# Performance work log

Hardware: AMD Instinct MI355X
Metric: run time of the kernel (lower is better)

The kernel has to match this reference:

```python
import jax, jax.numpy as jnp
import numpy as np

RADIUS = 0.08       # float radius -> patches_radius float branch
K = 32              # patch_size_source; spacing = 0 so topk k == K


def setup_inputs() -> dict:
    key = jax.random.key(0)
    k1, k2, k3, k4 = jax.random.split(key, 4)
    B, Ns, Nt = 2, 2048, 32768  # Nt = 32**3 (perfect cube for H_t reshape)
    return {
        "source": jax.random.normal(k1, (B, Ns, 3), dtype=jnp.float32),
        "target": jax.random.normal(k2, (B, Nt, 3), dtype=jnp.float32),
        "source_density": jax.random.uniform(k3, (B, Ns, 1), dtype=jnp.float32),
        "target_density": jax.random.uniform(k4, (B, Nt, 1), dtype=jnp.float32),
    }


def reference(source, target, source_density, target_density):
    B, Ns, _ = source.shape
    Nt = target.shape[1]

    # pairwise squared distances: (B, Nt, Ns)
    r0 = jnp.sum(target * target, axis=2, keepdims=True)            # B,Nt,1
    r1 = jnp.sum(source * source, axis=2, keepdims=True)            # B,Ns,1
    sq_dist = r0 - 2.0 * jnp.einsum('btc,bsc->bts', target, source) + jnp.swapaxes(r1, 1, 2)

    # computed in the original forward but never used downstream (dead value)
    _sq_dist_sel = sq_dist / (jnp.einsum('bti,bsi->bts', target_density, source_density) + 1e-8)

    # top-k nearest neighbors (spacing == 0)
    neg_vals, idx = jax.lax.top_k(-sq_dist, K)                      # B,Nt,K
    sq_pd = -neg_vals

    rad = RADIUS * jnp.ones((B, 1, 1), dtype=sq_dist.dtype)
    valid = (rad ** 2) >= sq_pd                                     # B,Nt,K (rad broadcast)
    idx = jnp.where(valid, idx, -1)

    b_idx = jnp.arange(B)[:, None, None]                            # B,1,1
    src_s = source / (rad + 1e-6)
    tgt_s = target / (rad + 1e-6)

    safe = jnp.maximum(idx, 0)
    patches = jnp.where(valid[..., None], src_s[b_idx, safe], 0.0)  # B,Nt,K,3
    patches = patches - tgt_s[:, :, None, :]
    density = jnp.where(valid[..., None], source_density[b_idx, safe], 0.0)  # B,Nt,K,1

    # gather of an all-ones (B,Ns) mask == validity indicator
    patch_valid = valid.astype(patches.dtype)
    patches_size = jnp.sum(patch_valid, axis=-1)                    # B,Nt

    patches_dist = jnp.sqrt(jnp.maximum(sq_pd, 1e-9)) / (rad + 1e-6)  # B,Nt,K

    mask_cnt = jnp.sum((idx < 0).astype(jnp.int32), axis=-1, keepdims=True)  # B,Nt,1
    weight_density = jnp.sum(density, axis=-2) / mask_cnt            # B,Nt,1

    H = int(round(Nt ** (1.0 / 3.0)))
    patches_idx = jnp.stack([jnp.broadcast_to(b_idx, (B, Nt, K)), idx], axis=-1)

    return (
        patches.reshape(B, H, H, H, K, 3),        # patches source
        patches_idx.reshape(B, H, H, H, K, 2),    # patches idx source
        patches_size,                              # patches size source
        rad,                                       # patches radius source
        patches_dist.reshape(B, H, H, H, K),       # patches dist source
        weight_density,                            # weighted density
    )
```

## Files before the change

kernel.cpp:

```cpp
#include <hip/hip_runtime.h>
#include <math.h>

constexpr int B_  = 2;
constexpr int NS_ = 2048;
constexpr int NT_ = 32768;
constexpr int K_  = 32;
#define RADIUS_F 0.08f

constexpr int TPB = 512;
constexpr int TGT_PER_WAVE = 8;
constexpr int TGT_PER_BLOCK = 8 * TGT_PER_WAVE;
constexpr int BLOCKS_PER_BATCH = NT_ / TGT_PER_BLOCK;
constexpr int NCHUNK = NS_ / 64;

constexpr int SZ_PATCH = B_ * NT_ * K_ * 3;
constexpr int SZ_IDX   = B_ * NT_ * K_ * 2;
constexpr int SZ_SIZE  = B_ * NT_;
constexpr int SZ_RAD   = B_;
constexpr int SZ_DIST  = B_ * NT_ * K_;
constexpr int O_PATCH = 0;
constexpr int O_IDX   = O_PATCH + SZ_PATCH;
constexpr int O_SIZE  = O_IDX + SZ_IDX;
constexpr int O_RAD   = O_SIZE + SZ_SIZE;
constexpr int O_DIST  = O_RAD + SZ_RAD;
constexpr int O_WD    = O_DIST + SZ_DIST;

constexpr unsigned long long tm_mask(int k, int j) {
    unsigned long long m = 0;
    for (int l = 0; l < 64; ++l)
        if (((l & k) == 0) == ((l & j) == 0)) m |= 1ull << l;
    return m;
}

__device__ __forceinline__ float readlane_f(float v, int l) {
    return __int_as_float(__builtin_amdgcn_readlane(__float_as_int(v), l));
}
__device__ __forceinline__ float bperm_f(int addr, float v) {
    return __int_as_float(__builtin_amdgcn_ds_bpermute(addr, __float_as_int(v)));
}
__device__ __forceinline__ float shr1_f(float v) {
    return __int_as_float(__builtin_amdgcn_update_dpp(0, __float_as_int(v),
                                                      0x138, 0xF, 0xF, true));
}
__device__ __forceinline__ float med3_vsv(float pv, int vbits, float lv) {
    float r;
    asm("v_med3_f32 %0, %1, %2, %3" : "=v"(r) : "v"(pv), "s"(vbits), "v"(lv));
    return r;
}
__device__ __forceinline__ float maxs_f(float p, int wbits) {
    float r;
    asm("v_max_f32 %0, %1, %2" : "=v"(r) : "s"(wbits), "v"(p));
    return r;
}
__device__ __forceinline__ float min3_f(float a, float b, float c) {
    float r;
    asm("v_min3_f32 %0, %1, %2, %3" : "=v"(r) : "v"(a), "v"(b), "v"(c));
    return r;
}
__device__ __forceinline__ void cnds(float& lv, float pv, unsigned long long keep) {
    float r;
    asm("v_cndmask_b32 %0, %2, %1, %3" : "=v"(r) : "v"(lv), "v"(pv), "s"(keep));
    lv = r;
}
__device__ __forceinline__ float dist_f(float tx, float ty, float tz, float r0, float4 sp) {
    float dot2 = __fadd_rn(__fadd_rn(__fmul_rn(tx, sp.x), __fmul_rn(ty, sp.y)), __fmul_rn(tz, sp.z));
    return __fadd_rn(__fadd_rn(r0, dot2), sp.w);
}

#define BSTG(LV, AJ, K, J) { \
    constexpr unsigned long long tm_ = tm_mask(K, J); \
    float pv_ = bperm_f(AJ, LV); \
    unsigned long long sm_ = __ballot((LV) < pv_); \
    cnds(LV, pv_, ~(sm_ ^ tm_)); \
}
#define S8(AJ, K, J) { BSTG(sa0, AJ, K, J) BSTG(sa1, AJ, K, J) BSTG(sa2, AJ, K, J) BSTG(sa3, AJ, K, J) \
                       BSTG(sb0, AJ, K, J) BSTG(sb1, AJ, K, J) BSTG(sb2, AJ, K, J) BSTG(sb3, AJ, K, J) }
#define C4(AJ, J) { BSTG(sa0, AJ, 128, J) BSTG(sa1, AJ, 128, J) BSTG(sa2, AJ, 128, J) BSTG(sa3, AJ, 128, J) }

#define REC(D, RV, RI, NV, BASE) { \
    unsigned long long mr_ = __ballot(r2f >= (D)); \
    while (mr_) { \
        int sl_ = (int)__builtin_ctzll(mr_); mr_ &= mr_ - 1; \
        float v_ = readlane_f(D, sl_); \
        if (lane == (NV)) { RV = v_; RI = (BASE) + sl_; } \
        ++(NV); \
    } \
}

#define INS2(D, LV, T) { \
    unsigned long long m_ = __ballot((D) < (T)); \
    while (m_) { \
        const int sl1_ = (int)__builtin_ctzll(m_); m_ &= m_ - 1; \
        const int b1_ = __builtin_amdgcn_readlane(__float_as_int(D), sl1_); \
        if (m_) { \
            const int sl2_ = (int)__builtin_ctzll(m_); m_ &= m_ - 1; \
            const int b2_ = __builtin_amdgcn_readlane(__float_as_int(D), sl2_); \
            const int w1_ = (b1_ < b2_) ? b1_ : b2_; \
            const int w2_ = (b1_ < b2_) ? b2_ : b1_; \
            float p1_ = shr1_f(LV); \
            float p2_ = shr1_f(p1_); \
            float t1_ = maxs_f(p1_, w1_); \
            float t2_ = maxs_f(p2_, w2_); \
            LV = min3_f(LV, t1_, t2_); \
        } else { \
            LV = med3_vsv(shr1_f(LV), b1_, LV); \
        } \
    } \
}

__device__ __forceinline__ void epilogue(
    float* __restrict__ out, const float* __restrict__ sden, const float4* ssp,
    int b, int tb, int lane,
    float lv, float rv, int ri, int nv,
    float tx, float ty, float tz)
{
    const float invdd = 1.0f / (RADIUS_F + 1e-6f);
    int vflag = 0; int vidx = -1; float dsum = 0.f; int vcnt = 0;
    const int sdb = b * NS_;
    const int nvc = (nv > 64) ? 64 : nv;
    for (int s = 0; s < nvc; ++s) {
        float vr = readlane_f(rv, s);
        int   ir = __builtin_amdgcn_readlane(ri, s);
        int rank = (int)__popcll(__ballot(lv < vr));
        for (int q = 0; q < s; ++q)
            rank += (readlane_f(rv, q) == vr) ? 1 : 0;
        if (rank < K_) {
            dsum += sden[sdb + ir];
            ++vcnt;
            if (lane == rank) { vflag = 1; vidx = ir; }
        }
    }
    float px = 0.f, py = 0.f, pz = 0.f;
    if (vflag) {
        float4 spv = ssp[vidx];
        px = spv.x * -0.5f;
        py = spv.y * -0.5f;
        pz = spv.z * -0.5f;
    }
    const float tsx = tx * invdd, tsy = ty * invdd, tsz = tz * invdd;
    if (lane < K_) {
        const int pb = tb * K_ + lane;
        float3 p3;
        p3.x = (vflag ? px * invdd : 0.0f) - tsx;
        p3.y = (vflag ? py * invdd : 0.0f) - tsy;
        p3.z = (vflag ? pz * invdd : 0.0f) - tsz;
        *reinterpret_cast<float3*>(&out[O_PATCH + pb * 3]) = p3;
        float2 ix;
        ix.x = (float)b;
        ix.y = (float)vidx;
        *reinterpret_cast<float2*>(&out[O_IDX + pb * 2]) = ix;
        out[O_DIST + tb * K_ + lane] = sqrtf(fmaxf(lv, 1e-9f)) * invdd;
    }
    if (lane == 0) {
        out[O_SIZE + tb] = (float)vcnt;
        out[O_WD + tb]   = dsum / (float)(K_ - vcnt);
    }
}

__global__ __launch_bounds__(TPB, 8) void group_points_kernel(
    const float* __restrict__ src,
    const float* __restrict__ tgt,
    const float* __restrict__ sden,
    float* __restrict__ out)
{
    __shared__ float4 s_sp[NS_];

    const int tid  = threadIdx.x;
    const int lane = tid & 63;
    const int wav  = tid >> 6;
    const int b    = blockIdx.x / BLOCKS_PER_BATCH;
    const int tile = blockIdx.x % BLOCKS_PER_BATCH;

    for (int j = tid; j < NS_; j += TPB) {
        const float* p = src + (b * NS_ + j) * 3;
        float x = p[0], y = p[1], z = p[2];
        float r1 = __fadd_rn(__fadd_rn(__fmul_rn(x, x), __fmul_rn(y, y)), __fmul_rn(z, z));
        s_sp[j] = make_float4(-2.f * x, -2.f * y, -2.f * z, r1);
    }
    if (blockIdx.x == 0 && tid == 0) {
        out[O_RAD + 0] = RADIUS_F;
        out[O_RAD + 1] = RADIUS_F;
    }
    __syncthreads();

    const float r2f = __fmul_rn(RADIUS_F, RADIUS_F);
    const int a1  = (lane ^ 1)  << 2;
    const int a2  = (lane ^ 2)  << 2;
    const int a4  = (lane ^ 4)  << 2;
    const int a8  = (lane ^ 8)  << 2;
    const int a16 = (lane ^ 16) << 2;
    const int a32 = (lane ^ 32) << 2;
    const int arev = (63 - lane) << 2;

    for (int gp = 0; gp < TGT_PER_WAVE / 4; ++gp) {
        const int t0 = tile * TGT_PER_BLOCK + wav * TGT_PER_WAVE + gp * 4;
        const int tb0 = b * NT_ + t0;
        const float* tp = tgt + tb0 * 3;
        const float tx0 = tp[0],  ty0 = tp[1],  tz0 = tp[2];
        const float tx1 = tp[3],  ty1 = tp[4],  tz1 = tp[5];
        const float tx2 = tp[6],  ty2 = tp[7],  tz2 = tp[8];
        const float tx3 = tp[9],  ty3 = tp[10], tz3 = tp[11];
        const float r00 = __fadd_rn(__fadd_rn(__fmul_rn(tx0, tx0), __fmul_rn(ty0, ty0)), __fmul_rn(tz0, tz0));
        const float r01 = __fadd_rn(__fadd_rn(__fmul_rn(tx1, tx1), __fmul_rn(ty1, ty1)), __fmul_rn(tz1, tz1));
        const float r02 = __fadd_rn(__fadd_rn(__fmul_rn(tx2, tx2), __fmul_rn(ty2, ty2)), __fmul_rn(tz2, tz2));
        const float r03 = __fadd_rn(__fadd_rn(__fmul_rn(tx3, tx3), __fmul_rn(ty3, ty3)), __fmul_rn(tz3, tz3));

        float rv0 = 0.f, rv1 = 0.f, rv2 = 0.f, rv3 = 0.f;
        int   ri0 = 0,   ri1 = 0,   ri2 = 0,   ri3 = 0;
        int   nv0 = 0,   nv1 = 0,   nv2 = 0,   nv3 = 0;

        float4 sp0 = s_sp[lane];
        float4 sp1 = s_sp[64 + lane];
        float sa0 = dist_f(tx0, ty0, tz0, r00, sp0);
        float sa1 = dist_f(tx1, ty1, tz1, r01, sp0);
        float sa2 = dist_f(tx2, ty2, tz2, r02, sp0);
        float sa3 = dist_f(tx3, ty3, tz3, r03, sp0);
        float sb0 = dist_f(tx0, ty0, tz0, r00, sp1);
        float sb1 = dist_f(tx1, ty1, tz1, r01, sp1);
        float sb2 = dist_f(tx2, ty2, tz2, r02, sp1);
        float sb3 = dist_f(tx3, ty3, tz3, r03, sp1);
        {
            float g8 = fminf(fminf(fminf(sa0, sa1), fminf(sa2, sa3)),
                             fminf(fminf(sb0, sb1), fminf(sb2, sb3)));
            if (__ballot(g8 <= r2f)) {
                REC(sa0, rv0, ri0, nv0, 0)  REC(sb0, rv0, ri0, nv0, 64)
                REC(sa1, rv1, ri1, nv1, 0)  REC(sb1, rv1, ri1, nv1, 64)
                REC(sa2, rv2, ri2, nv2, 0)  REC(sb2, rv2, ri2, nv2, 64)
                REC(sa3, rv3, ri3, nv3, 0)  REC(sb3, rv3, ri3, nv3, 64)
            }
        }
        S8(a1, 2, 1)
        S8(a2, 4, 2)   S8(a1, 4, 1)
        S8(a4, 8, 4)   S8(a2, 8, 2)   S8(a1, 8, 1)
        S8(a8, 16, 8)  S8(a4, 16, 4)  S8(a2, 16, 2)  S8(a1, 16, 1)
        S8(a16, 32, 16) S8(a8, 32, 8) S8(a4, 32, 4)  S8(a2, 32, 2)  S8(a1, 32, 1)
        S8(a32, 64, 32) S8(a16, 64, 16) S8(a8, 64, 8) S8(a4, 64, 4) S8(a2, 64, 2) S8(a1, 64, 1)
        sa0 = fminf(sa0, bperm_f(arev, sb0));
        sa1 = fminf(sa1, bperm_f(arev, sb1));
        sa2 = fminf(sa2, bperm_f(arev, sb2));
        sa3 = fminf(sa3, bperm_f(arev, sb3));
        C4(a32, 32) C4(a16, 16) C4(a8, 8) C4(a4, 4) C4(a2, 2) C4(a1, 1)
        float T0 = readlane_f(sa0, 31);
        float T1 = readlane_f(sa1, 31);
        float T2 = readlane_f(sa2, 31);
        float T3 = readlane_f(sa3, 31);

        for (int c = 2; c < NCHUNK; ++c) {
            float4 sp = s_sp[(c << 6) + lane];
            float d0 = dist_f(tx0, ty0, tz0, r00, sp);
            float d1 = dist_f(tx1, ty1, tz1, r01, sp);
            float d2 = dist_f(tx2, ty2, tz2, r02, sp);
            float d3 = dist_f(tx3, ty3, tz3, r03, sp);

            float g_ = fminf(fminf(d0, d1), fminf(d2, d3));
            if (__ballot(g_ <= r2f)) {
                const int base = c << 6;
                REC(d0, rv0, ri0, nv0, base)
                REC(d1, rv1, ri1, nv1, base)
                REC(d2, rv2, ri2, nv2, base)
                REC(d3, rv3, ri3, nv3, base)
            }

            INS2(d0, sa0, T0)
            INS2(d1, sa1, T1)
            INS2(d2, sa2, T2)
            INS2(d3, sa3, T3)
            if (c & 1) {
                T0 = readlane_f(sa0, 31);
                T1 = readlane_f(sa1, 31);
                T2 = readlane_f(sa2, 31);
                T3 = readlane_f(sa3, 31);
            }
        }

        epilogue(out, sden, s_sp, b, tb0,     lane, sa0, rv0, ri0, nv0, tx0, ty0, tz0);
        epilogue(out, sden, s_sp, b, tb0 + 1, lane, sa1, rv1, ri1, nv1, tx1, ty1, tz1);
        epilogue(out, sden, s_sp, b, tb0 + 2, lane, sa2, rv2, ri2, nv2, tx2, ty2, tz2);
        epilogue(out, sden, s_sp, b, tb0 + 3, lane, sa3, rv3, ri3, nv3, tx3, ty3, tz3);
    }
}

extern "C" void kernel_launch(void* const* d_in, const int* in_sizes, int n_in,
                              void* d_out, int out_size, void* d_ws, size_t ws_size,
                              hipStream_t stream) {
    const float* src  = (const float*)d_in[0];
    const float* tgt  = (const float*)d_in[1];
    const float* sden = (const float*)d_in[2];
    float* out = (float*)d_out;

    dim3 grid(B_ * BLOCKS_PER_BATCH);
    group_points_kernel<<<grid, TPB, 0, stream>>>(src, tgt, sden, out);
}
```

Before: 223.7 us.

## Use DPP min/max compare-exchange in bitonic sort and one target group per wave

Each wave now handles one group of 4 targets (TGT_PER_WAVE 8→4), which doubles the grid and removes the outer loop. The bitonic sort stages switch from a bpermute+ballot+cndmask exchange to a min/max+cndmask exchange using precomputed lane masks. Exchanges at distance 1 and 2 use DPP quad permutes instead of LDS bpermute. The threshold is also refreshed after every chunk instead of every other one, which tightens the insertion filter at the cost of more readlanes. The aim is shorter sort latency and more wave-level parallelism, at the risk of repeating the source-staging prologue in twice as many blocks.

```diff
diff --git a/kernel.cpp b/kernel.cpp
--- a/kernel.cpp
+++ b/kernel.cpp
@@ -8,7 +8,7 @@
 #define RADIUS_F 0.08f
 
 constexpr int TPB = 512;
-constexpr int TGT_PER_WAVE = 8;
+constexpr int TGT_PER_WAVE = 4;
 constexpr int TGT_PER_BLOCK = 8 * TGT_PER_WAVE;
 constexpr int BLOCKS_PER_BATCH = NT_ / TGT_PER_BLOCK;
 constexpr int NCHUNK = NS_ / 64;
@@ -42,6 +42,11 @@
     return __int_as_float(__builtin_amdgcn_update_dpp(0, __float_as_int(v),
                                                       0x138, 0xF, 0xF, true));
 }
+template<int CTRL>
+__device__ __forceinline__ float dppq_f(float v) {
+    return __int_as_float(__builtin_amdgcn_update_dpp(0, __float_as_int(v),
+                                                      CTRL, 0xF, 0xF, true));
+}
 __device__ __forceinline__ float med3_vsv(float pv, int vbits, float lv) {
     float r;
     asm("v_med3_f32 %0, %1, %2, %3" : "=v"(r) : "v"(pv), "s"(vbits), "v"(lv));
@@ -57,25 +62,34 @@
     asm("v_min3_f32 %0, %1, %2, %3" : "=v"(r) : "v"(a), "v"(b), "v"(c));
     return r;
 }
-__device__ __forceinline__ void cnds(float& lv, float pv, unsigned long long keep) {
+__device__ __forceinline__ float cndf(float a, float b, unsigned long long mask) {
     float r;
-    asm("v_cndmask_b32 %0, %2, %1, %3" : "=v"(r) : "v"(lv), "v"(pv), "s"(keep));
-    lv = r;
+    asm("v_cndmask_b32 %0, %2, %1, %3" : "=v"(r) : "v"(a), "v"(b), "s"(mask));
+    return r;
 }
 __device__ __forceinline__ float dist_f(float tx, float ty, float tz, float r0, float4 sp) {
     float dot2 = __fadd_rn(__fadd_rn(__fmul_rn(tx, sp.x), __fmul_rn(ty, sp.y)), __fmul_rn(tz, sp.z));
     return __fadd_rn(__fadd_rn(r0, dot2), sp.w);
 }
 
-#define BSTG(LV, AJ, K, J) { \
-    constexpr unsigned long long tm_ = tm_mask(K, J); \
-    float pv_ = bperm_f(AJ, LV); \
-    unsigned long long sm_ = __ballot((LV) < pv_); \
-    cnds(LV, pv_, ~(sm_ ^ tm_)); \
-}
-#define S8(AJ, K, J) { BSTG(sa0, AJ, K, J) BSTG(sa1, AJ, K, J) BSTG(sa2, AJ, K, J) BSTG(sa3, AJ, K, J) \
-                       BSTG(sb0, AJ, K, J) BSTG(sb1, AJ, K, J) BSTG(sb2, AJ, K, J) BSTG(sb3, AJ, K, J) }
-#define C4(AJ, J) { BSTG(sa0, AJ, 128, J) BSTG(sa1, AJ, 128, J) BSTG(sa2, AJ, 128, J) BSTG(sa3, AJ, 128, J) }
+#define CEXB(LV, AJ, M) { \
+    float p_ = bperm_f(AJ, LV); \
+    float mn_ = fminf(LV, p_); \
+    float mx_ = fmaxf(LV, p_); \
+    LV = cndf(mn_, mx_, M); \
+}
+#define CEXD(LV, CTRL, M) { \
+    float p_ = dppq_f<CTRL>(LV); \
+    float mn_ = fminf(LV, p_); \
+    float mx_ = fmaxf(LV, p_); \
+    LV = cndf(mn_, mx_, M); \
+}
+#define S8B(AJ, M) { CEXB(sa0, AJ, M) CEXB(sa1, AJ, M) CEXB(sa2, AJ, M) CEXB(sa3, AJ, M) \
+                     CEXB(sb0, AJ, M) CEXB(sb1, AJ, M) CEXB(sb2, AJ, M) CEXB(sb3, AJ, M) }
+#define S8D(CTRL, M) { CEXD(sa0, CTRL, M) CEXD(sa1, CTRL, M) CEXD(sa2, CTRL, M) CEXD(sa3, CTRL, M) \
+                       CEXD(sb0, CTRL, M) CEXD(sb1, CTRL, M) CEXD(sb2, CTRL, M) CEXD(sb3, CTRL, M) }
+#define C4B(AJ, M) { CEXB(sa0, AJ, M) CEXB(sa1, AJ, M) CEXB(sa2, AJ, M) CEXB(sa3, AJ, M) }
+#define C4D(CTRL, M) { CEXD(sa0, CTRL, M) CEXD(sa1, CTRL, M) CEXD(sa2, CTRL, M) CEXD(sa3, CTRL, M) }
 
 #define REC(D, RV, RI, NV, BASE) { \
     unsigned long long mr_ = __ballot(r2f >= (D)); \
@@ -184,100 +198,96 @@
     __syncthreads();
 
     const float r2f = __fmul_rn(RADIUS_F, RADIUS_F);
-    const int a1  = (lane ^ 1)  << 2;
-    const int a2  = (lane ^ 2)  << 2;
-    const int a4  = (lane ^ 4)  << 2;
-    const int a8  = (lane ^ 8)  << 2;
-    const int a16 = (lane ^ 16) << 2;
-    const int a32 = (lane ^ 32) << 2;
+    const int a4   = (lane ^ 4)  << 2;
+    const int a8   = (lane ^ 8)  << 2;
+    const int a16  = (lane ^ 16) << 2;
+    const int a32  = (lane ^ 32) << 2;
     const int arev = (63 - lane) << 2;
-
-    for (int gp = 0; gp < TGT_PER_WAVE / 4; ++gp) {
-        const int t0 = tile * TGT_PER_BLOCK + wav * TGT_PER_WAVE + gp * 4;
-        const int tb0 = b * NT_ + t0;
-        const float* tp = tgt + tb0 * 3;
-        const float tx0 = tp[0],  ty0 = tp[1],  tz0 = tp[2];
-        const float tx1 = tp[3],  ty1 = tp[4],  tz1 = tp[5];
-        const float tx2 = tp[6],  ty2 = tp[7],  tz2 = tp[8];
-        const float tx3 = tp[9],  ty3 = tp[10], tz3 = tp[11];
-        const float r00 = __fadd_rn(__fadd_rn(__fmul_rn(tx0, tx0), __fmul_rn(ty0, ty0)), __fmul_rn(tz0, tz0));
-        const float r01 = __fadd_rn(__fadd_rn(__fmul_rn(tx1, tx1), __fmul_rn(ty1, ty1)), __fmul_rn(tz1, tz1));
-        const float r02 = __fadd_rn(__fadd_rn(__fmul_rn(tx2, tx2), __fmul_rn(ty2, ty2)), __fmul_rn(tz2, tz2));
-        const float r03 = __fadd_rn(__fadd_rn(__fmul_rn(tx3, tx3), __fmul_rn(ty3, ty3)), __fmul_rn(tz3, tz3));
-
-        float rv0 = 0.f, rv1 = 0.f, rv2 = 0.f, rv3 = 0.f;
-        int   ri0 = 0,   ri1 = 0,   ri2 = 0,   ri3 = 0;
-        int   nv0 = 0,   nv1 = 0,   nv2 = 0,   nv3 = 0;
-
-        float4 sp0 = s_sp[lane];
-        float4 sp1 = s_sp[64 + lane];
-        float sa0 = dist_f(tx0, ty0, tz0, r00, sp0);
-        float sa1 = dist_f(tx1, ty1, tz1, r01, sp0);
-        float sa2 = dist_f(tx2, ty2, tz2, r02, sp0);
-        float sa3 = dist_f(tx3, ty3, tz3, r03, sp0);
-        float sb0 = dist_f(tx0, ty0, tz0, r00, sp1);
-        float sb1 = dist_f(tx1, ty1, tz1, r01, sp1);
-        float sb2 = dist_f(tx2, ty2, tz2, r02, sp1);
-        float sb3 = dist_f(tx3, ty3, tz3, r03, sp1);
-        {
-            float g8 = fminf(fminf(fminf(sa0, sa1), fminf(sa2, sa3)),
-                             fminf(fminf(sb0, sb1), fminf(sb2, sb3)));
-            if (__ballot(g8 <= r2f)) {
-                REC(sa0, rv0, ri0, nv0, 0)  REC(sb0, rv0, ri0, nv0, 64)
-                REC(sa1, rv1, ri1, nv1, 0)  REC(sb1, rv1, ri1, nv1, 64)
-                REC(sa2, rv2, ri2, nv2, 0)  REC(sb2, rv2, ri2, nv2, 64)
-                REC(sa3, rv3, ri3, nv3, 0)  REC(sb3, rv3, ri3, nv3, 64)
-            }
+    const unsigned long long M_2_1   = tm_mask(2, 1);
+    const unsigned long long M_4_2   = tm_mask(4, 2),  M_4_1  = tm_mask(4, 1);
+    const unsigned long long M_8_4   = tm_mask(8, 4),  M_8_2  = tm_mask(8, 2),  M_8_1  = tm_mask(8, 1);
+    const unsigned long long M_16_8  = tm_mask(16, 8), M_16_4 = tm_mask(16, 4), M_16_2 = tm_mask(16, 2), M_16_1 = tm_mask(16, 1);
+    const unsigned long long M_32_16 = tm_mask(32, 16), M_32_8 = tm_mask(32, 8), M_32_4 = tm_mask(32, 4), M_32_2 = tm_mask(32, 2), M_32_1 = tm_mask(32, 1);
+    const unsigned long long M_64_32 = tm_mask(64, 32), M_64_16 = tm_mask(64, 16), M_64_8 = tm_mask(64, 8), M_64_4 = tm_mask(64, 4), M_64_2 = tm_mask(64, 2), M_64_1 = tm_mask(64, 1);
+
+    const int t0 = tile * TGT_PER_BLOCK + wav * TGT_PER_WAVE;
+    const int tb0 = b * NT_ + t0;
+    const float* tp = tgt + tb0 * 3;
+    const float tx0 = tp[0],  ty0 = tp[1],  tz0 = tp[2];
+    const float tx1 = tp[3],  ty1 = tp[4],  tz1 = tp[5];
+    const float tx2 = tp[6],  ty2 = tp[7],  tz2 = tp[8];
+    const float tx3 = tp[9],  ty3 = tp[10], tz3 = tp[11];
+    const float r00 = __fadd_rn(__fadd_rn(__fmul_rn(tx0, tx0), __fmul_rn(ty0, ty0)), __fmul_rn(tz0, tz0));
+    const float r01 = __fadd_rn(__fadd_rn(__fmul_rn(tx1, tx1), __fmul_rn(ty1, ty1)), __fmul_rn(tz1, tz1));
+    const float r02 = __fadd_rn(__fadd_rn(__fmul_rn(tx2, tx2), __fmul_rn(ty2, ty2)), __fmul_rn(tz2, tz2));
+    const float r03 = __fadd_rn(__fadd_rn(__fmul_rn(tx3, tx3), __fmul_rn(ty3, ty3)), __fmul_rn(tz3, tz3));
+
+    float rv0 = 0.f, rv1 = 0.f, rv2 = 0.f, rv3 = 0.f;
+    int   ri0 = 0,   ri1 = 0,   ri2 = 0,   ri3 = 0;
+    int   nv0 = 0,   nv1 = 0,   nv2 = 0,   nv3 = 0;
+
+    float4 sp0 = s_sp[lane];
+    float4 sp1 = s_sp[64 + lane];
+    float sa0 = dist_f(tx0, ty0, tz0, r00, sp0);
+    float sa1 = dist_f(tx1, ty1, tz1, r01, sp0);
+    float sa2 = dist_f(tx2, ty2, tz2, r02, sp0);
+    float sa3 = dist_f(tx3, ty3, tz3, r03, sp0);
+    float sb0 = dist_f(tx0, ty0, tz0, r00, sp1);
+    float sb1 = dist_f(tx1, ty1, tz1, r01, sp1);
+    float sb2 = dist_f(tx2, ty2, tz2, r02, sp1);
+    float sb3 = dist_f(tx3, ty3, tz3, r03, sp1);
+    {
+        float g8 = fminf(fminf(fminf(sa0, sa1), fminf(sa2, sa3)),
+                         fminf(fminf(sb0, sb1), fminf(sb2, sb3)));
+        if (__ballot(g8 <= r2f)) {
+            REC(sa0, rv0, ri0, nv0, 0)  REC(sb0, rv0, ri0, nv0, 64)
+            REC(sa1, rv1, ri1, nv1, 0)  REC(sb1, rv1, ri1, nv1, 64)
+            REC(sa2, rv2, ri2, nv2, 0)  REC(sb2, rv2, ri2, nv2, 64)
+            REC(sa3, rv3, ri3, nv3, 0)  REC(sb3, rv3, ri3, nv3, 64)
         }
-        S8(a1, 2, 1)
-        S8(a2, 4, 2)   S8(a1, 4, 1)
-        S8(a4, 8, 4)   S8(a2, 8, 2)   S8(a1, 8, 1)
-        S8(a8, 16, 8)  S8(a4, 16, 4)  S8(a2, 16, 2)  S8(a1, 16, 1)
-        S8(a16, 32, 16) S8(a8, 32, 8) S8(a4, 32, 4)  S8(a2, 32, 2)  S8(a1, 32, 1)
-        S8(a32, 64, 32) S8(a16, 64, 16) S8(a8, 64, 8) S8(a4, 64, 4) S8(a2, 64, 2) S8(a1, 64, 1)
-        sa0 = fminf(sa0, bperm_f(arev, sb0));
-        sa1 = fminf(sa1, bperm_f(arev, sb1));
-        sa2 = fminf(sa2, bperm_f(arev, sb2));
-        sa3 = fminf(sa3, bperm_f(arev, sb3));
-        C4(a32, 32) C4(a16, 16) C4(a8, 8) C4(a4, 4) C4(a2, 2) C4(a1, 1)
-        float T0 = readlane_f(sa0, 31);
-        float T1 = readlane_f(sa1, 31);
-        float T2 = readlane_f(sa2, 31);
-        float T3 = readlane_f(sa3, 31);
-
-        for (int c = 2; c < NCHUNK; ++c) {
-            float4 sp = s_sp[(c << 6) + lane];
-            float d0 = dist_f(tx0, ty0, tz0, r00, sp);
-            float d1 = dist_f(tx1, ty1, tz1, r01, sp);
-            float d2 = dist_f(tx2, ty2, tz2, r02, sp);
-            float d3 = dist_f(tx3, ty3, tz3, r03, sp);
-
-            float g_ = fminf(fminf(d0, d1), fminf(d2, d3));
-            if (__ballot(g_ <= r2f)) {
-                const int base = c << 6;
-                REC(d0, rv0, ri0, nv0, base)
-                REC(d1, rv1, ri1, nv1, base)
-                REC(d2, rv2, ri2, nv2, base)
-                REC(d3, rv3, ri3, nv3, base)
-            }
-
-            INS2(d0, sa0, T0)
-            INS2(d1, sa1, T1)
-            INS2(d2, sa2, T2)
-            INS2(d3, sa3, T3)
-            if (c & 1) {
-                T0 = readlane_f(sa0, 31);
-                T1 = readlane_f(sa1, 31);
-                T2 = readlane_f(sa2, 31);
-                T3 = readlane_f(sa3, 31);
-            }
+    }
+    S8D(0xB1, M_2_1)
+    S8D(0x4E, M_4_2)   S8D(0xB1, M_4_1)
+    S8B(a4, M_8_4)     S8D(0x4E, M_8_2)   S8D(0xB1, M_8_1)
+    S8B(a8, M_16_8)    S8B(a4, M_16_4)    S8D(0x4E, M_16_2)  S8D(0xB1, M_16_1)
+    S8B(a16, M_32_16)  S8B(a8, M_32_8)    S8B(a4, M_32_4)    S8D(0x4E, M_32_2)  S8D(0xB1, M_32_1)
+    S8B(a32, M_64_32)  S8B(a16, M_64_16)  S8B(a8, M_64_8)    S8B(a4, M_64_4)    S8D(0x4E, M_64_2)  S8D(0xB1, M_64_1)
+    sa0 = fminf(sa0, bperm_f(arev, sb0));
+    sa1 = fminf(sa1, bperm_f(arev, sb1));
+    sa2 = fminf(sa2, bperm_f(arev, sb2));
+    sa3 = fminf(sa3, bperm_f(arev, sb3));
+    C4B(a32, M_64_32) C4B(a16, M_64_16) C4B(a8, M_64_8) C4B(a4, M_64_4) C4D(0x4E, M_64_2) C4D(0xB1, M_64_1)
+    float T0 = readlane_f(sa0, 31);
+    float T1 = readlane_f(sa1, 31);
+    float T2 = readlane_f(sa2, 31);
+    float T3 = readlane_f(sa3, 31);
+
+    for (int c = 2; c < NCHUNK; ++c) {
+        float4 sp = s_sp[(c << 6) + lane];
+        float d0 = dist_f(tx0, ty0, tz0, r00, sp);
+        float d1 = dist_f(tx1, ty1, tz1, r01, sp);
+        float d2 = dist_f(tx2, ty2, tz2, r02, sp);
+        float d3 = dist_f(tx3, ty3, tz3, r03, sp);
+
+        float g_ = fminf(fminf(d0, d1), fminf(d2, d3));
+        if (__ballot(g_ <= r2f)) {
+            const int base = c << 6;
+            REC(d0, rv0, ri0, nv0, base)
+            REC(d1, rv1, ri1, nv1, base)
+            REC(d2, rv2, ri2, nv2, base)
+            REC(d3, rv3, ri3, nv3, base)
         }
 
-        epilogue(out, sden, s_sp, b, tb0,     lane, sa0, rv0, ri0, nv0, tx0, ty0, tz0);
-        epilogue(out, sden, s_sp, b, tb0 + 1, lane, sa1, rv1, ri1, nv1, tx1, ty1, tz1);
-        epilogue(out, sden, s_sp, b, tb0 + 2, lane, sa2, rv2, ri2, nv2, tx2, ty2, tz2);
-        epilogue(out, sden, s_sp, b, tb0 + 3, lane, sa3, rv3, ri3, nv3, tx3, ty3, tz3);
-    }
+        INS2(d0, sa0, T0)  T0 = readlane_f(sa0, 31);
+        INS2(d1, sa1, T1)  T1 = readlane_f(sa1, 31);
+        INS2(d2, sa2, T2)  T2 = readlane_f(sa2, 31);
+        INS2(d3, sa3, T3)  T3 = readlane_f(sa3, 31);
+    }
+
+    epilogue(out, sden, s_sp, b, tb0,     lane, sa0, rv0, ri0, nv0, tx0, ty0, tz0);
+    epilogue(out, sden, s_sp, b, tb0 + 1, lane, sa1, rv1, ri1, nv1, tx1, ty1, tz1);
+    epilogue(out, sden, s_sp, b, tb0 + 2, lane, sa2, rv2, ri2, nv2, tx2, ty2, tz2);
+    epilogue(out, sden, s_sp, b, tb0 + 3, lane, sa3, rv3, ri3, nv3, tx3, ty3, tz3);
 }
 
 extern "C" void kernel_launch(void* const* d_in, const int* in_sizes, int n_in,
```

After: 195.5 us. 12.6% less time.
